# Kernel optimization log

Hardware: AMD Instinct MI355X
Metric: run time of the kernel (lower is better)

## Reference

```python
import jax, jax.numpy as jnp
import numpy as np

B, N, E = 2, 2048, 2048
H, G, D = 16, 4, 128          # num_heads, num_kv_groups, head_dim = E // H
HID = 4 * E                    # GeGLU hidden width
EPS = 1e-6


def setup_inputs() -> dict:
    key = jax.random.key(0)
    ks = jax.random.split(key, 8)
    g = lambda k, shape: jax.random.normal(k, shape, jnp.float32) * 0.02
    return {
        "x": jax.random.normal(ks[0], (B, N, E), jnp.float32),
        "wq": g(ks[1], (E, H * D)),
        "wk": g(ks[2], (E, G * D)),
        "wv": g(ks[3], (E, G * D)),
        "wo": g(ks[4], (H * D, E)),
        "w1": g(ks[5], (E, 2 * HID)),   # GeGLU in-proj (value | gate)
        "w2": g(ks[6], (HID, E)),       # GeGLU out-proj
        "norm1_w": jnp.ones((E,), jnp.float32),
        "norm2_w": jnp.ones((E,), jnp.float32),
    }


def _rope_cos_sin(n, d, dtype):
    inv_freq = 1.0 / (10000.0 ** (jnp.arange(0, d, 2, dtype=jnp.float32) / d))
    freqs = jnp.arange(n, dtype=jnp.float32)[:, None] * inv_freq[None, :]  # [n, d/2]
    emb = jnp.concatenate([freqs, freqs], axis=-1)                          # [n, d]
    return jnp.cos(emb).astype(dtype), jnp.sin(emb).astype(dtype)


def _rotate_half(t):
    d2 = t.shape[-1] // 2
    return jnp.concatenate([-t[..., d2:], t[..., :d2]], axis=-1)


def _apply_rope(t, cos, sin):
    # t: [b, h, n, d]; cos/sin: [n, d]
    return t * cos + _rotate_half(t) * sin


def _rmsnorm(x, w):
    var = jnp.mean(jnp.square(x), axis=-1, keepdims=True)
    return x * jax.lax.rsqrt(var + EPS) * w


def reference(x, wq, wk, wv, wo, w1, w2, norm1_w, norm2_w):
    b, n, _ = x.shape
    # q = k = v = x reshaped into heads (pre-projection, as in source)
    qkv = x.reshape(b, n, H, D).transpose(0, 2, 1, 3)  # [b, H, n, D]
    cos, sin = _rope_cos_sin(n, D, x.dtype)
    q_r = _apply_rope(qkv, cos, sin)
    k_r = _apply_rope(qkv, cos, sin)
    # flatten back to [b, n, E]
    q_flat = q_r.transpose(0, 2, 1, 3).reshape(b, n, E)
    k_flat = k_r.transpose(0, 2, 1, 3).reshape(b, n, E)
    v_flat = x  # v untouched by RoPE; flatten == x

    # Grouped-query attention with internal projections
    qh = (q_flat @ wq).reshape(b, n, H, D).transpose(0, 2, 1, 3)       # [b, H, n, D]
    kh = (k_flat @ wk).reshape(b, n, G, D)                              # [b, n, G, D]
    vh = (v_flat @ wv).reshape(b, n, G, D)
    kh = jnp.repeat(kh, H // G, axis=2).transpose(0, 2, 1, 3)           # [b, H, n, D]
    vh = jnp.repeat(vh, H // G, axis=2).transpose(0, 2, 1, 3)

    scale = 1.0 / np.sqrt(D)
    scores = jnp.einsum('bhqd,bhkd->bhqk', qh, kh) * scale
    attn = jax.nn.softmax(scores, axis=-1)                               # [b, H, n, n]
    ctx = jnp.einsum('bhqk,bhkd->bhqd', attn, vh)
    attn_out = ctx.transpose(0, 2, 1, 3).reshape(b, n, H * D) @ wo      # [b, n, E]

    x1 = _rmsnorm(x + attn_out, norm1_w)

    # GeGLU FFN
    uv = x1 @ w1
    u, gate = jnp.split(uv, 2, axis=-1)
    fc = (u * jax.nn.gelu(gate)) @ w2

    x2 = _rmsnorm(x1 + fc, norm2_w)
    return (x2, (k_flat, v_flat), attn)
```

## Files before the change

kernel.cpp:

```cpp
#include <hip/hip_runtime.h>
#include <hip/hip_bf16.h>


using f32x4  = __attribute__((ext_vector_type(4))) float;
using bf16x8 = __attribute__((ext_vector_type(8))) short;
using bf16x4 = __attribute__((ext_vector_type(4))) short;
using u16x4  = __attribute__((ext_vector_type(4))) unsigned short;

#define DEV __device__ __forceinline__

#define ASYNC16(lds, g)                                                        \
  __builtin_amdgcn_global_load_lds(                                           \
      (const __attribute__((address_space(1))) void*)(g),                      \
      (__attribute__((address_space(3))) void*)(lds), 16, 0, 0)

DEV unsigned short f2bf(float f) {
  unsigned int u = __float_as_uint(f);
  return (unsigned short)((u + 0x7fffu + ((u >> 16) & 1u)) >> 16);
}
DEV float bf2f(unsigned short h) {
  return __uint_as_float(((unsigned int)h) << 16);
}

DEV float waveRedSum(float v) {
#pragma unroll
  for (int o = 32; o; o >>= 1) v += __shfl_xor(v, o);
  return v;
}

__global__ __launch_bounds__(256) void kconvT(const float* __restrict__ in,
                                              unsigned short* __restrict__ out,
                                              int K, int N) {
  __shared__ float tile[32][33];
  int bx = blockIdx.x * 32;
  int by = blockIdx.y * 32;
  int tx = threadIdx.x & 31;
  int ty = threadIdx.x >> 5;
#pragma unroll
  for (int i = 0; i < 32; i += 8)
    tile[ty + i][tx] = in[(size_t)(by + ty + i) * N + bx + tx];
  __syncthreads();
#pragma unroll
  for (int i = 0; i < 32; i += 8)
    out[(size_t)(bx + ty + i) * K + by + tx] = f2bf(tile[tx][ty + i]);
}

__global__ __launch_bounds__(256) void krope(const float* __restrict__ x,
                                             float* __restrict__ kout,
                                             float* __restrict__ vout,
                                             unsigned short* __restrict__ xq,
                                             unsigned short* __restrict__ xb) {
  int idx = blockIdx.x * 256 + threadIdx.x;
  int f  = idx & 63;
  int h  = (idx >> 6) & 15;
  int bn = idx >> 10;
  int n  = bn & 2047;
  size_t base = (size_t)bn * 2048 + h * 128;
  float inv = exp2f((float)f * (-13.287712379549449f / 64.0f));
  float ang = (float)n * inv;
  float c = cosf(ang), s = sinf(ang);
  float a = x[base + f], b = x[base + f + 64];
  float k1 = a * c - b * s;
  float k2 = b * c + a * s;
  kout[base + f]      = k1;
  kout[base + f + 64] = k2;
  xq[base + f]      = f2bf(k1);
  xq[base + f + 64] = f2bf(k2);
  vout[base + f]      = a;
  vout[base + f + 64] = b;
  xb[base + f]      = f2bf(a);
  xb[base + f + 64] = f2bf(b);
}

__global__ __launch_bounds__(256) void krms1(const float* __restrict__ x,
                                             const float* __restrict__ ao,
                                             const float* __restrict__ w,
                                             unsigned short* __restrict__ x1b) {
  size_t row = blockIdx.x;
  const f32x4* xp = (const f32x4*)(x + row * 2048);
  const f32x4* ap = (const f32x4*)(ao + row * 2048);
  int tid = threadIdx.x;
  f32x4 t0 = xp[tid * 2] + ap[tid * 2];
  f32x4 t1 = xp[tid * 2 + 1] + ap[tid * 2 + 1];
  float ss = 0.f;
#pragma unroll
  for (int i = 0; i < 4; ++i) ss += t0[i] * t0[i] + t1[i] * t1[i];
  ss = waveRedSum(ss);
  __shared__ float red[4];
  int wid = tid >> 6, lane = tid & 63;
  if (!lane) red[wid] = ss;
  __syncthreads();
  ss = red[0] + red[1] + red[2] + red[3];
  float rr = rsqrtf(ss * (1.0f / 2048.0f) + 1e-6f);
  const f32x4* wp = (const f32x4*)w;
  f32x4 w0 = wp[tid * 2], w1 = wp[tid * 2 + 1];
  u16x4 o0, o1;
#pragma unroll
  for (int i = 0; i < 4; ++i) {
    o0[i] = f2bf(t0[i] * rr * w0[i]);
    o1[i] = f2bf(t1[i] * rr * w1[i]);
  }
  u16x4* op = (u16x4*)(x1b + row * 2048);
  op[tid * 2] = o0;
  op[tid * 2 + 1] = o1;
}

__global__ __launch_bounds__(256) void krms2(const unsigned short* __restrict__ x1b,
                                             const unsigned short* __restrict__ fc,
                                             const float* __restrict__ w,
                                             float* __restrict__ out) {
  size_t row = blockIdx.x;
  const u16x4* xp = (const u16x4*)(x1b + row * 2048);
  const u16x4* fp = (const u16x4*)(fc + row * 2048);
  int tid = threadIdx.x;
  u16x4 a0 = xp[tid * 2], a1 = xp[tid * 2 + 1];
  u16x4 b0 = fp[tid * 2], b1 = fp[tid * 2 + 1];
  f32x4 t0, t1;
#pragma unroll
  for (int i = 0; i < 4; ++i) {
    t0[i] = bf2f(a0[i]) + bf2f(b0[i]);
    t1[i] = bf2f(a1[i]) + bf2f(b1[i]);
  }
  float ss = 0.f;
#pragma unroll
  for (int i = 0; i < 4; ++i) ss += t0[i] * t0[i] + t1[i] * t1[i];
  ss = waveRedSum(ss);
  __shared__ float red[4];
  int wid = tid >> 6, lane = tid & 63;
  if (!lane) red[wid] = ss;
  __syncthreads();
  ss = red[0] + red[1] + red[2] + red[3];
  float rr = rsqrtf(ss * (1.0f / 2048.0f) + 1e-6f);
  const f32x4* wp = (const f32x4*)w;
  f32x4 w0 = wp[tid * 2], w1 = wp[tid * 2 + 1];
  f32x4* op = (f32x4*)(out + row * 2048);
  op[tid * 2]     = t0 * rr * w0;
  op[tid * 2 + 1] = t1 * rr * w1;
}

template <bool OUT_BF16, bool TRANS_OUT>
__global__ __launch_bounds__(256, 2) void gemm_bt(
    const unsigned short* __restrict__ A, const unsigned short* __restrict__ Bt,
    void* __restrict__ C_, int K, int lda, int ldb, int ldc, float alpha) {
  __shared__ unsigned short As[128 * 32];
  __shared__ unsigned short Bs[128 * 32];
  const int tid = threadIdx.x;
  const int bm0 = blockIdx.y * 128, bn0 = blockIdx.x * 128;

  f32x4 acc[4][4] = {};

  const int lane = tid & 63, wid = tid >> 6;
  const int wr = wid >> 1, wc = wid & 1;
  const int lr = lane & 15, kq = lane >> 4;
  const int srow = tid >> 2;
  const int scol = (tid & 3) * 8;
  unsigned short* AsW = As + tid * 8;
  unsigned short* BsW = Bs + tid * 8;

  for (int kt = 0; kt < K; kt += 32) {
    ASYNC16(AsW,        A + (size_t)(bm0 + srow)      * lda + kt + scol);
    ASYNC16(AsW + 2048, A + (size_t)(bm0 + srow + 64) * lda + kt + scol);
    ASYNC16(BsW,        Bt + (size_t)(bn0 + srow)      * ldb + kt + scol);
    ASYNC16(BsW + 2048, Bt + (size_t)(bn0 + srow + 64) * ldb + kt + scol);
    __syncthreads();
    bf16x8 afr[4], bfr[4];
#pragma unroll
    for (int i = 0; i < 4; ++i)
      afr[i] = *(const bf16x8*)&As[(wr * 64 + i * 16 + lr) * 32 + kq * 8];
#pragma unroll
    for (int j = 0; j < 4; ++j)
      bfr[j] = *(const bf16x8*)&Bs[(wc * 64 + j * 16 + lr) * 32 + kq * 8];
#pragma unroll
    for (int i = 0; i < 4; ++i)
#pragma unroll
      for (int j = 0; j < 4; ++j)
        acc[i][j] = __builtin_amdgcn_mfma_f32_16x16x32_bf16(afr[i], bfr[j],
                                                            acc[i][j], 0, 0, 0);
    __syncthreads();
  }

#pragma unroll
  for (int i = 0; i < 4; ++i)
#pragma unroll
    for (int j = 0; j < 4; ++j) {
      int rowb = bm0 + wr * 64 + i * 16 + kq * 4;
      int col = bn0 + wc * 64 + j * 16 + lr;
#pragma unroll
      for (int r = 0; r < 4; ++r) {
        float v = acc[i][j][r] * alpha;
        size_t idx = TRANS_OUT ? ((size_t)col * ldc + (rowb + r))
                               : ((size_t)(rowb + r) * ldc + col);
        if constexpr (OUT_BF16)
          ((unsigned short*)C_)[idx] = f2bf(v);
        else
          ((float*)C_)[idx] = v;
      }
    }
}

__global__ __launch_bounds__(512, 4) void kattn(
    const unsigned short* __restrict__ qh,
    const unsigned short* __restrict__ kh,
    const unsigned short* __restrict__ vT,
    float* __restrict__ attn,
    unsigned short* __restrict__ ctx) {
  __shared__ __align__(16) char U[65536];
  __shared__ __align__(16) char Vb[16384];
  float* redm = (float*)Vb;
  float* reds = redm + 128;

  const int tid = threadIdx.x;
  const int lane = tid & 63, w = tid >> 6;
  const int lr = lane & 15, kq = lane >> 4;
  const int bid = blockIdx.x;
  const int g8 = bid & 7;
  const int j  = bid >> 3;
  const int bz = g8 >> 2;
  const int gz = g8 & 3;
  const int hz = gz * 4 + (j & 3);
  const int q0 = (j >> 2) << 4;
  const int z  = bz * 16 + hz;

  const unsigned short* Aq =
      qh + ((size_t)(bz * 2048 + q0 + lr) * 2048 + hz * 128);
  bf16x8 qfr[4];
#pragma unroll
  for (int kk = 0; kk < 4; ++kk)
    qfr[kk] = *(const bf16x8*)(Aq + kk * 32 + kq * 8);

  const unsigned short* Kb =
      kh + ((size_t)(bz * 2048) * 512 + gz * 128);
  int krow[4], kcs[4];
#pragma unroll
  for (int R = 0; R < 4; ++R) {
    int idx = R * 64 + lane;
    krow[R] = idx >> 4;
    kcs[R] = (idx & 15) ^ (krow[R] & 7);
  }
  auto stageK = [&](int buf, int t) {
#pragma unroll
    for (int R = 0; R < 4; ++R)
      ASYNC16(U + buf * 32768 + w * 4096 + (R * 64 + lane) * 16,
              Kb + (size_t)(t * 128 + w * 16 + krow[R]) * 512 + kcs[R] * 8);
  };

  f32x4 acc[16];
#pragma unroll
  for (int t = 0; t < 16; ++t) acc[t] = f32x4{0.f, 0.f, 0.f, 0.f};

  stageK(0, 0);
  stageK(1, 1);
#pragma unroll
  for (int t = 0; t < 16; ++t) {
    if (t < 15) asm volatile("s_waitcnt vmcnt(4)" ::: "memory");
    else        asm volatile("s_waitcnt vmcnt(0)" ::: "memory");
    __builtin_amdgcn_sched_barrier(0);
    const char* Kw = U + (t & 1) * 32768 + w * 4096;
    bf16x8 kfr[4];
#pragma unroll
    for (int kk = 0; kk < 4; ++kk) {
      int cch = (kk * 4 + kq) ^ (lr & 7);
      kfr[kk] = *(const bf16x8*)(Kw + lr * 256 + cch * 16);
    }
    asm volatile("s_waitcnt lgkmcnt(0)" ::: "memory");
    __builtin_amdgcn_sched_barrier(0);
    if (t + 2 < 16) stageK(t & 1, t + 2);
#pragma unroll
    for (int kk = 0; kk < 4; ++kk)
      acc[t] = __builtin_amdgcn_mfma_f32_16x16x32_bf16(kfr[kk], qfr[kk],
                                                       acc[t], 0, 0, 0);
  }

  const float scale = 0.08838834764831845f;
  float mx = -3.4e38f;
#pragma unroll
  for (int t = 0; t < 16; ++t) {
    acc[t] *= scale;
#pragma unroll
    for (int r = 0; r < 4; ++r) mx = fmaxf(mx, acc[t][r]);
  }
  mx = fmaxf(mx, __shfl_xor(mx, 16));
  mx = fmaxf(mx, __shfl_xor(mx, 32));
  if (kq == 0) redm[w * 16 + lr] = mx;
  __syncthreads();
  mx = redm[lr];
#pragma unroll
  for (int ww = 1; ww < 8; ++ww) mx = fmaxf(mx, redm[ww * 16 + lr]);

  float sm = 0.f;
#pragma unroll
  for (int t = 0; t < 16; ++t) {
#pragma unroll
    for (int r = 0; r < 4; ++r) {
      float e = __expf(acc[t][r] - mx);
      acc[t][r] = e;
      sm += e;
    }
  }
  sm += __shfl_xor(sm, 16);
  sm += __shfl_xor(sm, 32);
  if (kq == 0) reds[w * 16 + lr] = sm;
  __syncthreads();
  float smt = reds[lr];
#pragma unroll
  for (int ww = 1; ww < 8; ++ww) smt += reds[ww * 16 + lr];
  float inv = 1.0f / smt;

  float* arow = attn + (((size_t)z * 2048 + q0 + lr) * 2048);
#pragma unroll
  for (int t = 0; t < 16; ++t) {
    int key = t * 128 + w * 16 + kq * 4;
    f32x4 p = acc[t] * inv;
    *(f32x4*)(arow + key) = p;
    bf16x4 pb;
#pragma unroll
    for (int r = 0; r < 4; ++r) pb[r] = (short)f2bf(p[r]);
    int c8 = key >> 3;
    *(bf16x4*)(U + lr * 4096 + ((c8 ^ (lr & 7)) << 4) + ((key & 7) << 1)) = pb;
  }
  __syncthreads();

  const unsigned short* Bv = vT + (size_t)gz * 524288 + bz * 2048;
  const int d0 = w * 16;
  const int vd = lane >> 2;
  const int vcs = (lane & 3) ^ (vd & 3);
  auto stageV = [&](int buf, int t) {
    ASYNC16(Vb + buf * 8192 + w * 1024 + lane * 16,
            Bv + (size_t)(d0 + vd) * 4096 + t * 32 + vcs * 8);
  };

  f32x4 cfr = {};
  stageV(0, 0);
  stageV(1, 1);
#pragma unroll
  for (int t = 0; t < 64; ++t) {
    if (t < 63) asm volatile("s_waitcnt vmcnt(1)" ::: "memory");
    else        asm volatile("s_waitcnt vmcnt(0)" ::: "memory");
    __builtin_amdgcn_sched_barrier(0);
    int c8 = t * 4 + kq;
    bf16x8 pfr = *(const bf16x8*)(U + lr * 4096 + ((c8 ^ (lr & 7)) << 4));
    const char* Vw = Vb + (t & 1) * 8192 + w * 1024;
    bf16x8 vfr = *(const bf16x8*)(Vw + lr * 64 + ((kq ^ (lr & 3)) << 4));
    asm volatile("s_waitcnt lgkmcnt(0)" ::: "memory");
    __builtin_amdgcn_sched_barrier(0);
    if (t + 2 < 64) stageV(t & 1, t + 2);
    cfr = __builtin_amdgcn_mfma_f32_16x16x32_bf16(pfr, vfr, cfr, 0, 0, 0);
  }
#pragma unroll
  for (int r = 0; r < 4; ++r) {
    int q = kq * 4 + r;
    ctx[((size_t)(bz * 2048 + q0 + q) * 2048) + hz * 128 + d0 + lr] =
        f2bf(cfr[r]);
  }
}

template <bool OUT_BF16>
__global__ __launch_bounds__(512, 1) void gemm256(
    const unsigned short* __restrict__ A, const unsigned short* __restrict__ Bt,
    void* __restrict__ C_, int K, int lda, int ldb, int ldc) {
  __shared__ unsigned short As[3][256 * 64];
  __shared__ unsigned short Bs[3][128 * 64];
  const int tid = threadIdx.x;
  const int bm0 = blockIdx.y * 256, bn0 = blockIdx.x * 128;
  const int lane = tid & 63, wid = tid >> 6;
  const int wr = wid >> 2, wc = wid & 3;
  const int lr = lane & 15, kq = lane >> 4;

  f32x4 acc[8][2] = {};

  int sArow[4], sAcc[4], sBrow[2], sBcc[2];
#pragma unroll
  for (int R = 0; R < 4; ++R) {
    int c = R * 512 + tid;
    sArow[R] = c >> 3;
    sAcc[R]  = (c & 7) ^ (sArow[R] & 7);
  }
#pragma unroll
  for (int R = 0; R < 2; ++R) {
    int c = R * 512 + tid;
    sBrow[R] = c >> 3;
    sBcc[R]  = (c & 7) ^ (sBrow[R] & 7);
  }

  auto stage = [&](int buf, int k0) {
#pragma unroll
    for (int R = 0; R < 4; ++R)
      ASYNC16(&As[buf][(R * 512 + tid) * 8],
              A + (size_t)(bm0 + sArow[R]) * lda + k0 + sAcc[R] * 8);
#pragma unroll
    for (int R = 0; R < 2; ++R)
      ASYNC16(&Bs[buf][(R * 512 + tid) * 8],
              Bt + (size_t)(bn0 + sBrow[R]) * ldb + k0 + sBcc[R] * 8);
  };

  const int NT = K >> 6;
  stage(0, 0);
  stage(1, 64);
  int cur = 0;
  for (int t = 0; t < NT; ++t) {
    if (t + 1 < NT) asm volatile("s_waitcnt vmcnt(6)" ::: "memory");
    else            asm volatile("s_waitcnt vmcnt(0)" ::: "memory");
    __builtin_amdgcn_sched_barrier(0);
    __builtin_amdgcn_s_barrier();
    __builtin_amdgcn_sched_barrier(0);
    {
      int nbuf = cur + 2 >= 3 ? cur - 1 : cur + 2;
      if (t + 2 < NT) stage(nbuf, (t + 2) << 6);
    }
    const unsigned short* Ac = As[cur];
    const unsigned short* Bc = Bs[cur];
    bf16x8 afr0[8], bfr0[2];
#pragma unroll
    for (int i = 0; i < 8; ++i) {
      int row = wr * 128 + i * 16 + lr;
      afr0[i] = *(const bf16x8*)&Ac[(row * 8 + (kq ^ (row & 7))) * 8];
    }
#pragma unroll
    for (int j2 = 0; j2 < 2; ++j2) {
      int brow = wc * 32 + j2 * 16 + lr;
      bfr0[j2] = *(const bf16x8*)&Bc[(brow * 8 + (kq ^ (brow & 7))) * 8];
    }
    __builtin_amdgcn_s_setprio(1);
#pragma unroll
    for (int j2 = 0; j2 < 2; ++j2)
#pragma unroll
      for (int i = 0; i < 8; ++i)
        acc[i][j2] = __builtin_amdgcn_mfma_f32_16x16x32_bf16(afr0[i], bfr0[j2],
                                                             acc[i][j2], 0, 0, 0);
    __builtin_amdgcn_s_setprio(0);
    bf16x8 afr1[8], bfr1[2];
#pragma unroll
    for (int i = 0; i < 8; ++i) {
      int row = wr * 128 + i * 16 + lr;
      afr1[i] = *(const bf16x8*)&Ac[(row * 8 + ((4 + kq) ^ (row & 7))) * 8];
    }
#pragma unroll
    for (int j2 = 0; j2 < 2; ++j2) {
      int brow = wc * 32 + j2 * 16 + lr;
      bfr1[j2] = *(const bf16x8*)&Bc[(brow * 8 + ((4 + kq) ^ (brow & 7))) * 8];
    }
    __builtin_amdgcn_s_setprio(1);
#pragma unroll
    for (int j2 = 0; j2 < 2; ++j2)
#pragma unroll
      for (int i = 0; i < 8; ++i)
        acc[i][j2] = __builtin_amdgcn_mfma_f32_16x16x32_bf16(afr1[i], bfr1[j2],
                                                             acc[i][j2], 0, 0, 0);
    __builtin_amdgcn_s_setprio(0);
    asm volatile("s_waitcnt lgkmcnt(0)" ::: "memory");
    __builtin_amdgcn_sched_barrier(0);
    cur = cur + 1 >= 3 ? 0 : cur + 1;
  }

#pragma unroll
  for (int i = 0; i < 8; ++i)
#pragma unroll
    for (int j = 0; j < 2; ++j) {
      int rowb = bm0 + wr * 128 + i * 16 + kq * 4;
      int col = bn0 + wc * 32 + j * 16 + lr;
#pragma unroll
      for (int r = 0; r < 4; ++r) {
        if constexpr (OUT_BF16)
          ((unsigned short*)C_)[(size_t)(rowb + r) * ldc + col] = f2bf(acc[i][j][r]);
        else
          ((float*)C_)[(size_t)(rowb + r) * ldc + col] = acc[i][j][r];
      }
    }
}

__global__ __launch_bounds__(512, 2) void gemm_geglu256(
    const unsigned short* __restrict__ A, const unsigned short* __restrict__ B1,
    const unsigned short* __restrict__ B2, unsigned short* __restrict__ H_,
    int K, int lda, int ldb, int ldc) {
  __shared__ unsigned short As[2][256 * 64];
  __shared__ unsigned short B1s[2][128 * 64];
  __shared__ unsigned short B2s[2][128 * 64];
  const int tid = threadIdx.x;
  const int bm0 = blockIdx.y * 256, bn0 = blockIdx.x * 128;
  const int lane = tid & 63, wid = tid >> 6;
  const int wr = wid >> 2, wc = wid & 3;
  const int lr = lane & 15, kq = lane >> 4;

  f32x4 accu[8][2] = {};
  f32x4 accg[8][2] = {};

  int sArow[4], sAcc[4], sBrow[2], sBcc[2];
#pragma unroll
  for (int R = 0; R < 4; ++R) {
    int c = R * 512 + tid;
    sArow[R] = c >> 3;
    sAcc[R]  = (c & 7) ^ (sArow[R] & 7);
  }
#pragma unroll
  for (int R = 0; R < 2; ++R) {
    int c = R * 512 + tid;
    sBrow[R] = c >> 3;
    sBcc[R]  = (c & 7) ^ (sBrow[R] & 7);
  }

  auto stage = [&](int buf, int k0) {
#pragma unroll
    for (int R = 0; R < 4; ++R)
      ASYNC16(&As[buf][(R * 512 + tid) * 8],
              A + (size_t)(bm0 + sArow[R]) * lda + k0 + sAcc[R] * 8);
#pragma unroll
    for (int R = 0; R < 2; ++R)
      ASYNC16(&B1s[buf][(R * 512 + tid) * 8],
              B1 + (size_t)(bn0 + sBrow[R]) * ldb + k0 + sBcc[R] * 8);
#pragma unroll
    for (int R = 0; R < 2; ++R)
      ASYNC16(&B2s[buf][(R * 512 + tid) * 8],
              B2 + (size_t)(bn0 + sBrow[R]) * ldb + k0 + sBcc[R] * 8);
  };

  const int NT = K >> 6;
  stage(0, 0);
  stage(1, 64);
  int cur = 0;
  for (int t = 0; t < NT; ++t) {
    if (t + 1 < NT) asm volatile("s_waitcnt vmcnt(8)" ::: "memory");
    else            asm volatile("s_waitcnt vmcnt(0)" ::: "memory");
    __builtin_amdgcn_sched_barrier(0);
    __builtin_amdgcn_s_barrier();
    __builtin_amdgcn_sched_barrier(0);
    const unsigned short* Ac = As[cur];
    const unsigned short* B1c = B1s[cur];
    const unsigned short* B2c = B2s[cur];
    bf16x8 afr0[8], b10[2], b20[2];
#pragma unroll
    for (int i = 0; i < 8; ++i) {
      int row = wr * 128 + i * 16 + lr;
      afr0[i] = *(const bf16x8*)&Ac[(row * 8 + (kq ^ (row & 7))) * 8];
    }
#pragma unroll
    for (int j2 = 0; j2 < 2; ++j2) {
      int brow = wc * 32 + j2 * 16 + lr;
      b10[j2] = *(const bf16x8*)&B1c[(brow * 8 + (kq ^ (brow & 7))) * 8];
      b20[j2] = *(const bf16x8*)&B2c[(brow * 8 + (kq ^ (brow & 7))) * 8];
    }
    __builtin_amdgcn_s_setprio(1);
#pragma unroll
    for (int j2 = 0; j2 < 2; ++j2)
#pragma unroll
      for (int i = 0; i < 8; ++i) {
        accu[i][j2] = __builtin_amdgcn_mfma_f32_16x16x32_bf16(afr0[i], b10[j2],
                                                              accu[i][j2], 0, 0, 0);
        accg[i][j2] = __builtin_amdgcn_mfma_f32_16x16x32_bf16(afr0[i], b20[j2],
                                                              accg[i][j2], 0, 0, 0);
      }
    __builtin_amdgcn_s_setprio(0);
    bf16x8 afr1[8], b11[2], b21[2];
#pragma unroll
    for (int i = 0; i < 8; ++i) {
      int row = wr * 128 + i * 16 + lr;
      afr1[i] = *(const bf16x8*)&Ac[(row * 8 + ((4 + kq) ^ (row & 7))) * 8];
    }
#pragma unroll
    for (int j2 = 0; j2 < 2; ++j2) {
      int brow = wc * 32 + j2 * 16 + lr;
      b11[j2] = *(const bf16x8*)&B1c[(brow * 8 + ((4 + kq) ^ (brow & 7))) * 8];
      b21[j2] = *(const bf16x8*)&B2c[(brow * 8 + ((4 + kq) ^ (brow & 7))) * 8];
    }
    asm volatile("s_waitcnt lgkmcnt(0)" ::: "memory");
    __builtin_amdgcn_sched_barrier(0);
    __builtin_amdgcn_s_barrier();
    __builtin_amdgcn_sched_barrier(0);
    if (t + 2 < NT) stage(cur, (t + 2) << 6);
    __builtin_amdgcn_s_setprio(1);
#pragma unroll
    for (int j2 = 0; j2 < 2; ++j2)
#pragma unroll
      for (int i = 0; i < 8; ++i) {
        accu[i][j2] = __builtin_amdgcn_mfma_f32_16x16x32_bf16(afr1[i], b11[j2],
                                                              accu[i][j2], 0, 0, 0);
        accg[i][j2] = __builtin_amdgcn_mfma_f32_16x16x32_bf16(afr1[i], b21[j2],
                                                              accg[i][j2], 0, 0, 0);
      }
    __builtin_amdgcn_s_setprio(0);
    cur ^= 1;
  }

#pragma unroll
  for (int i = 0; i < 8; ++i)
#pragma unroll
    for (int j = 0; j < 2; ++j) {
      int rowb = bm0 + wr * 128 + i * 16 + kq * 4;
      int col = bn0 + wc * 32 + j * 16 + lr;
#pragma unroll
      for (int r = 0; r < 4; ++r) {
        float u = accu[i][j][r];
        float g = accg[i][j][r];
        float tv = tanhf(0.7978845608028654f * (g + 0.044715f * g * g * g));
        float hv = u * 0.5f * g * (1.0f + tv);
        H_[(size_t)(rowb + r) * ldc + col] = f2bf(hv);
      }
    }
}

extern "C" void kernel_launch(void* const* d_in, const int* in_sizes, int n_in,
                              void* d_out, int out_size, void* d_ws, size_t ws_size,
                              hipStream_t stream) {
  const float* x   = (const float*)d_in[0];
  const float* wq  = (const float*)d_in[1];
  const float* wk  = (const float*)d_in[2];
  const float* wv  = (const float*)d_in[3];
  const float* wo  = (const float*)d_in[4];
  const float* w1  = (const float*)d_in[5];
  const float* w2  = (const float*)d_in[6];
  const float* n1w = (const float*)d_in[7];
  const float* n2w = (const float*)d_in[8];

  float* out    = (float*)d_out;
  float* x2_out = out;
  float* k_out  = out + 8388608;
  float* v_out  = out + 16777216;
  float* attn   = out + 25165824;

  char* ws = (char*)d_ws;
  unsigned short* wqT  = (unsigned short*)(ws + 0);
  unsigned short* wkT  = (unsigned short*)(ws + 8388608);
  unsigned short* wvT  = (unsigned short*)(ws + 10485760);
  unsigned short* woT  = (unsigned short*)(ws + 12582912);
  unsigned short* w1T  = (unsigned short*)(ws + 20971520);
  unsigned short* w2T  = (unsigned short*)(ws + 88080384);
  unsigned short* qh   = (unsigned short*)(ws + 121634816);
  unsigned short* kh   = (unsigned short*)(ws + 138412032);
  unsigned short* vhT  = (unsigned short*)(ws + 142606336);
  unsigned short* ctx  = (unsigned short*)(ws + 146800640);
  float*          ao   = (float*)(ws + 163577856);
  unsigned short* hbuf = (unsigned short*)(ws + 121634816);
  unsigned short* x1b  = (unsigned short*)(ws + 197132288);
  unsigned short* fc   = (unsigned short*)(ws + 213909504);

  unsigned short* xb = (unsigned short*)attn;
  unsigned short* xq = xb + 8388608;

  dim3 blk(256);
  dim3 blk512(512);

  kconvT<<<dim3(64, 64), blk, 0, stream>>>(wq, wqT, 2048, 2048);
  kconvT<<<dim3(16, 64), blk, 0, stream>>>(wk, wkT, 2048, 512);
  kconvT<<<dim3(16, 64), blk, 0, stream>>>(wv, wvT, 2048, 512);
  kconvT<<<dim3(64, 64), blk, 0, stream>>>(wo, woT, 2048, 2048);
  kconvT<<<dim3(512, 64), blk, 0, stream>>>(w1, w1T, 2048, 16384);
  kconvT<<<dim3(64, 256), blk, 0, stream>>>(w2, w2T, 8192, 2048);

  krope<<<16384, blk, 0, stream>>>(x, k_out, v_out, xq, xb);

  gemm256<true><<<dim3(16, 16), blk512, 0, stream>>>(
      xq, wqT, qh, 2048, 2048, 2048, 2048);
  gemm_bt<true, false><<<dim3(4, 32), blk, 0, stream>>>(
      xq, wkT, kh, 2048, 2048, 2048, 512, 1.0f);
  gemm_bt<true, true><<<dim3(4, 32), blk, 0, stream>>>(
      xb, wvT, vhT, 2048, 2048, 2048, 4096, 1.0f);

  kattn<<<dim3(4096), blk512, 0, stream>>>(qh, kh, vhT, attn, ctx);

  gemm256<false><<<dim3(16, 16), blk512, 0, stream>>>(
      ctx, woT, (void*)ao, 2048, 2048, 2048, 2048);
  krms1<<<4096, blk, 0, stream>>>(x, ao, n1w, x1b);
  gemm_geglu256<<<dim3(64, 16), blk512, 0, stream>>>(
      x1b, w1T, w1T + 16777216, hbuf, 2048, 2048, 2048, 8192);
  gemm256<true><<<dim3(16, 16), blk512, 0, stream>>>(
      hbuf, w2T, fc, 8192, 8192, 8192, 2048);
  krms2<<<4096, blk, 0, stream>>>(x1b, fc, n2w, x2_out);
}
```

Baseline: 1.087 ms.

## Load V directly to registers in attention; double-buffer GEMM for two blocks/CU

In the attention kernel, the PV stage now reads V fragments straight from global memory into four rotating registers instead of staging them through a dedicated LDS buffer. This frees that 16KB of shared memory, which could allow more resident blocks per CU. The GEMM drops from triple to double buffering, cutting LDS to 96KB so launch bounds can request two blocks per CU. Prefetch of tile t+2 now goes into the current buffer after an extra barrier placed mid-iteration. The trade-off is less load/compute overlap in both kernels and uncoalesced-ish global V reads.

```diff
diff --git a/kernel.cpp b/kernel.cpp
--- a/kernel.cpp
+++ b/kernel.cpp
@@ -205,9 +205,7 @@
     float* __restrict__ attn,
     unsigned short* __restrict__ ctx) {
   __shared__ __align__(16) char U[65536];
-  __shared__ __align__(16) char Vb[16384];
-  float* redm = (float*)Vb;
-  float* reds = redm + 128;
+  __shared__ float redm[128], reds[128];
 
   const int tid = threadIdx.x;
   const int lane = tid & 63, w = tid >> 6;
@@ -322,29 +320,38 @@
 
   const unsigned short* Bv = vT + (size_t)gz * 524288 + bz * 2048;
   const int d0 = w * 16;
-  const int vd = lane >> 2;
-  const int vcs = (lane & 3) ^ (vd & 3);
-  auto stageV = [&](int buf, int t) {
-    ASYNC16(Vb + buf * 8192 + w * 1024 + lane * 16,
-            Bv + (size_t)(d0 + vd) * 4096 + t * 32 + vcs * 8);
-  };
-
+  const unsigned short* Vp = Bv + (size_t)(d0 + lr) * 4096 + kq * 8;
+  bf16x8 vr0 = *(const bf16x8*)(Vp);
+  bf16x8 vr1 = *(const bf16x8*)(Vp + 32);
+  bf16x8 vr2 = *(const bf16x8*)(Vp + 64);
+  bf16x8 vr3 = *(const bf16x8*)(Vp + 96);
   f32x4 cfr = {};
-  stageV(0, 0);
-  stageV(1, 1);
-#pragma unroll
-  for (int t = 0; t < 64; ++t) {
-    if (t < 63) asm volatile("s_waitcnt vmcnt(1)" ::: "memory");
-    else        asm volatile("s_waitcnt vmcnt(0)" ::: "memory");
-    __builtin_amdgcn_sched_barrier(0);
-    int c8 = t * 4 + kq;
-    bf16x8 pfr = *(const bf16x8*)(U + lr * 4096 + ((c8 ^ (lr & 7)) << 4));
-    const char* Vw = Vb + (t & 1) * 8192 + w * 1024;
-    bf16x8 vfr = *(const bf16x8*)(Vw + lr * 64 + ((kq ^ (lr & 3)) << 4));
-    asm volatile("s_waitcnt lgkmcnt(0)" ::: "memory");
-    __builtin_amdgcn_sched_barrier(0);
-    if (t + 2 < 64) stageV(t & 1, t + 2);
-    cfr = __builtin_amdgcn_mfma_f32_16x16x32_bf16(pfr, vfr, cfr, 0, 0, 0);
+#pragma unroll
+  for (int tt = 0; tt < 64; tt += 4) {
+    {
+      bf16x8 p = *(const bf16x8*)(U + lr * 4096 +
+                                  (((tt * 4 + kq) ^ (lr & 7)) << 4));
+      cfr = __builtin_amdgcn_mfma_f32_16x16x32_bf16(p, vr0, cfr, 0, 0, 0);
+      if (tt + 4 < 64) vr0 = *(const bf16x8*)(Vp + (tt + 4) * 32);
+    }
+    {
+      bf16x8 p = *(const bf16x8*)(U + lr * 4096 +
+                                  ((((tt + 1) * 4 + kq) ^ (lr & 7)) << 4));
+      cfr = __builtin_amdgcn_mfma_f32_16x16x32_bf16(p, vr1, cfr, 0, 0, 0);
+      if (tt + 5 < 64) vr1 = *(const bf16x8*)(Vp + (tt + 5) * 32);
+    }
+    {
+      bf16x8 p = *(const bf16x8*)(U + lr * 4096 +
+                                  ((((tt + 2) * 4 + kq) ^ (lr & 7)) << 4));
+      cfr = __builtin_amdgcn_mfma_f32_16x16x32_bf16(p, vr2, cfr, 0, 0, 0);
+      if (tt + 6 < 64) vr2 = *(const bf16x8*)(Vp + (tt + 6) * 32);
+    }
+    {
+      bf16x8 p = *(const bf16x8*)(U + lr * 4096 +
+                                  ((((tt + 3) * 4 + kq) ^ (lr & 7)) << 4));
+      cfr = __builtin_amdgcn_mfma_f32_16x16x32_bf16(p, vr3, cfr, 0, 0, 0);
+      if (tt + 7 < 64) vr3 = *(const bf16x8*)(Vp + (tt + 7) * 32);
+    }
   }
 #pragma unroll
   for (int r = 0; r < 4; ++r) {
@@ -355,11 +362,11 @@
 }
 
 template <bool OUT_BF16>
-__global__ __launch_bounds__(512, 1) void gemm256(
+__global__ __launch_bounds__(512, 2) void gemm256(
     const unsigned short* __restrict__ A, const unsigned short* __restrict__ Bt,
     void* __restrict__ C_, int K, int lda, int ldb, int ldc) {
-  __shared__ unsigned short As[3][256 * 64];
-  __shared__ unsigned short Bs[3][128 * 64];
+  __shared__ unsigned short As[2][256 * 64];
+  __shared__ unsigned short Bs[2][128 * 64];
   const int tid = threadIdx.x;
   const int bm0 = blockIdx.y * 256, bn0 = blockIdx.x * 128;
   const int lane = tid & 63, wid = tid >> 6;
@@ -403,10 +410,6 @@
     __builtin_amdgcn_sched_barrier(0);
     __builtin_amdgcn_s_barrier();
     __builtin_amdgcn_sched_barrier(0);
-    {
-      int nbuf = cur + 2 >= 3 ? cur - 1 : cur + 2;
-      if (t + 2 < NT) stage(nbuf, (t + 2) << 6);
-    }
     const unsigned short* Ac = As[cur];
     const unsigned short* Bc = Bs[cur];
     bf16x8 afr0[8], bfr0[2];
@@ -439,6 +442,11 @@
       int brow = wc * 32 + j2 * 16 + lr;
       bfr1[j2] = *(const bf16x8*)&Bc[(brow * 8 + ((4 + kq) ^ (brow & 7))) * 8];
     }
+    asm volatile("s_waitcnt lgkmcnt(0)" ::: "memory");
+    __builtin_amdgcn_sched_barrier(0);
+    __builtin_amdgcn_s_barrier();
+    __builtin_amdgcn_sched_barrier(0);
+    if (t + 2 < NT) stage(cur, (t + 2) << 6);
     __builtin_amdgcn_s_setprio(1);
 #pragma unroll
     for (int j2 = 0; j2 < 2; ++j2)
@@ -447,9 +455,7 @@
         acc[i][j2] = __builtin_amdgcn_mfma_f32_16x16x32_bf16(afr1[i], bfr1[j2],
                                                              acc[i][j2], 0, 0, 0);
     __builtin_amdgcn_s_setprio(0);
-    asm volatile("s_waitcnt lgkmcnt(0)" ::: "memory");
-    __builtin_amdgcn_sched_barrier(0);
-    cur = cur + 1 >= 3 ? 0 : cur + 1;
+    cur ^= 1;
   }
 
 #pragma unroll
```

Measured after the change: 1.171 ms. 7.7% more time.
